# Optimization experiments

Measured on AMD Instinct MI355X. Metric: run time of the kernel, lower is better.

The kernel has to match this reference:

```python
import jax, jax.numpy as jnp
import numpy as np

SMOOTH = 1.0  # smooth=1
P = 2         # denominator power


def setup_inputs() -> dict:
    key = jax.random.key(0)
    k1, k2, k3 = jax.random.split(key, 3)
    N, C, H, W = 16, 4, 768, 768
    predict = jax.random.normal(k1, (N, C, H, W), dtype=jnp.float32)
    target = jax.random.randint(k2, (N, H, W), 0, C, dtype=jnp.int32)
    masks = jax.random.randint(k3, (N, H, W), 0, 2, dtype=jnp.int32)
    return {"predict": predict, "target": target, "masks": masks}


def reference(predict, target, masks):
    N, C = predict.shape[0], predict.shape[1]
    # softmax over class dim, flatten spatial dims -> [N, C, M]
    sm = jax.nn.softmax(predict, axis=1).reshape(N, C, -1)
    # one-hot target -> [N, C, M] (equivalent to make_one_hot scatter)
    onehot = jax.nn.one_hot(target.reshape(N, -1), C, dtype=predict.dtype)
    onehot = jnp.transpose(onehot, (0, 2, 1))  # [N, C, M]
    # predict[masks < 1] = target[...]: overwrite prediction where mask is off
    m = (masks.reshape(N, 1, -1) >= 1)  # broadcast over C
    p_eff = jnp.where(m, sm, onehot)
    # BinaryDiceLoss per class, vectorized over C
    num = jnp.sum(p_eff * onehot, axis=2) + SMOOTH            # [N, C]
    den = jnp.sum(p_eff ** P + onehot ** P, axis=2) + SMOOTH  # [N, C]
    loss = 1.0 - num / den                                    # [N, C]
    per_class = jnp.mean(loss, axis=0)  # reduction='mean' over batch
    # ignore_index=[] -> sum over all classes, divide by C
    return jnp.sum(per_class) / C
```

## Files before the change

kernel.cpp:

```cpp
#include <hip/hip_runtime.h>

typedef float f4 __attribute__((ext_vector_type(4)));
typedef int   i4 __attribute__((ext_vector_type(4)));

constexpr int NB = 16;
constexpr int NC = 4;
constexpr int HW = 768 * 768;
constexpr int M4 = HW / 4;
constexpr int BLOCKS_PER_IMG = 144;

__global__ __launch_bounds__(256) void dice_partial(
    const float* __restrict__ predict,
    const int*   __restrict__ target,
    const int*   __restrict__ masks,
    float*       __restrict__ ws)
{
    const int n = blockIdx.y;
    const float* p = predict + (size_t)n * NC * HW;
    const f4* pc0 = (const f4*)(p);
    const f4* pc1 = (const f4*)(p + (size_t)HW);
    const f4* pc2 = (const f4*)(p + (size_t)2 * HW);
    const f4* pc3 = (const f4*)(p + (size_t)3 * HW);
    const i4* tg  = (const i4*)(target + (size_t)n * HW);
    const i4* mk  = (const i4*)(masks  + (size_t)n * HW);

    float num0 = 0.f, num1 = 0.f, num2 = 0.f, num3 = 0.f;
    float den0 = 0.f, den1 = 0.f, den2 = 0.f, den3 = 0.f;

    const int stride = gridDim.x * blockDim.x;
    for (int v = blockIdx.x * blockDim.x + threadIdx.x; v < M4; v += stride) {
        f4 a = pc0[v];
        f4 b = pc1[v];
        f4 c = pc2[v];
        f4 d = pc3[v];
        i4 t = tg[v];
        i4 m = mk[v];

#pragma unroll
        for (int j = 0; j < 4; ++j) {
            const float x0 = a[j], x1 = b[j], x2 = c[j], x3 = d[j];
            const int   tt = t[j];
            const bool  on = (m[j] >= 1);

            const float mx  = fmaxf(fmaxf(x0, x1), fmaxf(x2, x3));
            const float e0  = __expf(x0 - mx);
            const float e1  = __expf(x1 - mx);
            const float e2  = __expf(x2 - mx);
            const float e3  = __expf(x3 - mx);
            const float inv = 1.0f / (e0 + e1 + e2 + e3);
            const float s0  = e0 * inv, s1 = e1 * inv, s2 = e2 * inv, s3 = e3 * inv;

            const float oh0 = (tt == 0) ? 1.0f : 0.0f;
            const float oh1 = (tt == 1) ? 1.0f : 0.0f;
            const float oh2 = (tt == 2) ? 1.0f : 0.0f;
            const float oh3 = (tt == 3) ? 1.0f : 0.0f;

            const float f0 = on ? s0 : oh0;
            const float f1 = on ? s1 : oh1;
            const float f2 = on ? s2 : oh2;
            const float f3 = on ? s3 : oh3;

            num0 += f0 * oh0;  den0 += f0 * f0 + oh0;
            num1 += f1 * oh1;  den1 += f1 * f1 + oh1;
            num2 += f2 * oh2;  den2 += f2 * f2 + oh2;
            num3 += f3 * oh3;  den3 += f3 * f3 + oh3;
        }
    }

#pragma unroll
    for (int off = 32; off > 0; off >>= 1) {
        num0 += __shfl_down(num0, off);
        num1 += __shfl_down(num1, off);
        num2 += __shfl_down(num2, off);
        num3 += __shfl_down(num3, off);
        den0 += __shfl_down(den0, off);
        den1 += __shfl_down(den1, off);
        den2 += __shfl_down(den2, off);
        den3 += __shfl_down(den3, off);
    }

    __shared__ float sred[4][8];
    const int wid  = threadIdx.x >> 6;
    const int lane = threadIdx.x & 63;
    if (lane == 0) {
        sred[wid][0] = num0; sred[wid][1] = num1; sred[wid][2] = num2; sred[wid][3] = num3;
        sred[wid][4] = den0; sred[wid][5] = den1; sred[wid][6] = den2; sred[wid][7] = den3;
    }
    __syncthreads();
    if (threadIdx.x < 8) {
        const float s = sred[0][threadIdx.x] + sred[1][threadIdx.x]
                      + sred[2][threadIdx.x] + sred[3][threadIdx.x];
        atomicAdd(&ws[n * 8 + threadIdx.x], s);
    }
}

__global__ void dice_final(const float* __restrict__ ws, float* __restrict__ out)
{
    const int i = threadIdx.x;
    const int n = i >> 2;
    const int c = i & 3;
    const float num = ws[n * 8 + c]     + 1.0f;
    const float den = ws[n * 8 + 4 + c] + 1.0f;
    float l = 1.0f - num / den;

#pragma unroll
    for (int off = 32; off > 0; off >>= 1) l += __shfl_down(l, off);

    if (i == 0) out[0] = l * (1.0f / (NB * NC));
}

extern "C" void kernel_launch(void* const* d_in, const int* in_sizes, int n_in,
                              void* d_out, int out_size, void* d_ws, size_t ws_size,
                              hipStream_t stream) {
    const float* predict = (const float*)d_in[0];
    const int*   target  = (const int*)d_in[1];
    const int*   masks   = (const int*)d_in[2];
    float*       out     = (float*)d_out;
    float*       ws      = (float*)d_ws;

    hipMemsetAsync(ws, 0, NB * 8 * sizeof(float), stream);

    dim3 grid(BLOCKS_PER_IMG, NB);
    dice_partial<<<grid, 256, 0, stream>>>(predict, target, masks, ws);
    dice_final<<<1, 64, 0, stream>>>(ws, out);
}
```

Baseline: 46.29 us.

## Batch all loads up front and replace atomics with per-block partial reduction

Replaces the grid-stride loop with a fully unrolled four-chunk pass that issues every vector load before any compute, raising memory-level parallelism. Per-block sums are written to distinct workspace slots instead of atomically accumulated, so the memset launch is dropped and the final kernel reduces the partials. This hard-codes the problem size to exactly four strides per thread and costs more registers.

```diff
diff --git a/kernel.cpp b/kernel.cpp
--- a/kernel.cpp
+++ b/kernel.cpp
@@ -8,6 +8,46 @@
 constexpr int HW = 768 * 768;
 constexpr int M4 = HW / 4;
 constexpr int BLOCKS_PER_IMG = 144;
+constexpr int CHUNK_STRIDE = BLOCKS_PER_IMG * 256;
+constexpr int ITERS = 4;
+
+
+__device__ __forceinline__ void accum_chunk(
+    const f4& a, const f4& b, const f4& c, const f4& d,
+    const i4& t, const i4& m,
+    float& num0, float& num1, float& num2, float& num3,
+    float& den0, float& den1, float& den2, float& den3)
+{
+#pragma unroll
+    for (int j = 0; j < 4; ++j) {
+        const float x0 = a[j], x1 = b[j], x2 = c[j], x3 = d[j];
+        const int   tt = t[j];
+        const bool  on = (m[j] >= 1);
+
+        const float mx  = fmaxf(fmaxf(x0, x1), fmaxf(x2, x3));
+        const float e0  = __expf(x0 - mx);
+        const float e1  = __expf(x1 - mx);
+        const float e2  = __expf(x2 - mx);
+        const float e3  = __expf(x3 - mx);
+        const float inv = 1.0f / (e0 + e1 + e2 + e3);
+        const float s0  = e0 * inv, s1 = e1 * inv, s2 = e2 * inv, s3 = e3 * inv;
+
+        const float oh0 = (tt == 0) ? 1.0f : 0.0f;
+        const float oh1 = (tt == 1) ? 1.0f : 0.0f;
+        const float oh2 = (tt == 2) ? 1.0f : 0.0f;
+        const float oh3 = (tt == 3) ? 1.0f : 0.0f;
+
+        const float f0 = on ? s0 : oh0;
+        const float f1 = on ? s1 : oh1;
+        const float f2 = on ? s2 : oh2;
+        const float f3 = on ? s3 : oh3;
+
+        num0 += f0 * oh0;  den0 += f0 * f0 + oh0;
+        num1 += f1 * oh1;  den1 += f1 * f1 + oh1;
+        num2 += f2 * oh2;  den2 += f2 * f2 + oh2;
+        num3 += f3 * oh3;  den3 += f3 * f3 + oh3;
+    }
+}
 
 __global__ __launch_bounds__(256) void dice_partial(
     const float* __restrict__ predict,
@@ -24,48 +64,27 @@
     const i4* tg  = (const i4*)(target + (size_t)n * HW);
     const i4* mk  = (const i4*)(masks  + (size_t)n * HW);
 
+    const int base = blockIdx.x * 256 + threadIdx.x;
+
+    f4 a[ITERS], b[ITERS], c[ITERS], d[ITERS];
+    i4 t[ITERS], m[ITERS];
+#pragma unroll
+    for (int k = 0; k < ITERS; ++k) {
+        const int v = base + k * CHUNK_STRIDE;
+        a[k] = pc0[v];
+        b[k] = pc1[v];
+        c[k] = pc2[v];
+        d[k] = pc3[v];
+        t[k] = tg[v];
+        m[k] = mk[v];
+    }
+
     float num0 = 0.f, num1 = 0.f, num2 = 0.f, num3 = 0.f;
     float den0 = 0.f, den1 = 0.f, den2 = 0.f, den3 = 0.f;
-
-    const int stride = gridDim.x * blockDim.x;
-    for (int v = blockIdx.x * blockDim.x + threadIdx.x; v < M4; v += stride) {
-        f4 a = pc0[v];
-        f4 b = pc1[v];
-        f4 c = pc2[v];
-        f4 d = pc3[v];
-        i4 t = tg[v];
-        i4 m = mk[v];
-
 #pragma unroll
-        for (int j = 0; j < 4; ++j) {
-            const float x0 = a[j], x1 = b[j], x2 = c[j], x3 = d[j];
-            const int   tt = t[j];
-            const bool  on = (m[j] >= 1);
-
-            const float mx  = fmaxf(fmaxf(x0, x1), fmaxf(x2, x3));
-            const float e0  = __expf(x0 - mx);
-            const float e1  = __expf(x1 - mx);
-            const float e2  = __expf(x2 - mx);
-            const float e3  = __expf(x3 - mx);
-            const float inv = 1.0f / (e0 + e1 + e2 + e3);
-            const float s0  = e0 * inv, s1 = e1 * inv, s2 = e2 * inv, s3 = e3 * inv;
-
-            const float oh0 = (tt == 0) ? 1.0f : 0.0f;
-            const float oh1 = (tt == 1) ? 1.0f : 0.0f;
-            const float oh2 = (tt == 2) ? 1.0f : 0.0f;
-            const float oh3 = (tt == 3) ? 1.0f : 0.0f;
-
-            const float f0 = on ? s0 : oh0;
-            const float f1 = on ? s1 : oh1;
-            const float f2 = on ? s2 : oh2;
-            const float f3 = on ? s3 : oh3;
-
-            num0 += f0 * oh0;  den0 += f0 * f0 + oh0;
-            num1 += f1 * oh1;  den1 += f1 * f1 + oh1;
-            num2 += f2 * oh2;  den2 += f2 * f2 + oh2;
-            num3 += f3 * oh3;  den3 += f3 * f3 + oh3;
-        }
-    }
+    for (int k = 0; k < ITERS; ++k)
+        accum_chunk(a[k], b[k], c[k], d[k], t[k], m[k],
+                    num0, num1, num2, num3, den0, den1, den2, den3);
 
 #pragma unroll
     for (int off = 32; off > 0; off >>= 1) {
@@ -90,23 +109,32 @@
     if (threadIdx.x < 8) {
         const float s = sred[0][threadIdx.x] + sred[1][threadIdx.x]
                       + sred[2][threadIdx.x] + sred[3][threadIdx.x];
-        atomicAdd(&ws[n * 8 + threadIdx.x], s);
+        ws[(n * 8 + threadIdx.x) * BLOCKS_PER_IMG + blockIdx.x] = s;
     }
 }
 
-__global__ void dice_final(const float* __restrict__ ws, float* __restrict__ out)
+__global__ __launch_bounds__(128) void dice_final(
+    const float* __restrict__ ws, float* __restrict__ out)
 {
+    __shared__ float ssum[128];
     const int i = threadIdx.x;
-    const int n = i >> 2;
-    const int c = i & 3;
-    const float num = ws[n * 8 + c]     + 1.0f;
-    const float den = ws[n * 8 + 4 + c] + 1.0f;
-    float l = 1.0f - num / den;
+    float s = 0.f;
+    const float* row = ws + (size_t)i * BLOCKS_PER_IMG;
+#pragma unroll 4
+    for (int k = 0; k < BLOCKS_PER_IMG; ++k) s += row[k];
+    ssum[i] = s;
+    __syncthreads();
 
+    if (i < 64) {
+        const int n = i >> 2;
+        const int c = i & 3;
+        const float num = ssum[n * 8 + c]     + 1.0f;
+        const float den = ssum[n * 8 + 4 + c] + 1.0f;
+        float l = 1.0f - num / den;
 #pragma unroll
-    for (int off = 32; off > 0; off >>= 1) l += __shfl_down(l, off);
-
-    if (i == 0) out[0] = l * (1.0f / (NB * NC));
+        for (int off = 32; off > 0; off >>= 1) l += __shfl_down(l, off);
+        if (i == 0) out[0] = l * (1.0f / (NB * NC));
+    }
 }
 
 extern "C" void kernel_launch(void* const* d_in, const int* in_sizes, int n_in,
@@ -118,9 +146,7 @@
     float*       out     = (float*)d_out;
     float*       ws      = (float*)d_ws;
 
-    hipMemsetAsync(ws, 0, NB * 8 * sizeof(float), stream);
-
     dim3 grid(BLOCKS_PER_IMG, NB);
     dice_partial<<<grid, 256, 0, stream>>>(predict, target, masks, ws);
-    dice_final<<<1, 64, 0, stream>>>(ws, out);
+    dice_final<<<1, 128, 0, stream>>>(ws, out);
 }
```

After: 47.30 us. 1.02x slower.
